# Performance work log

Hardware: AMD Instinct MI355X
Metric: run time of the kernel (lower is better)

## Reference

```python
import jax, jax.numpy as jnp
import numpy as np
import math

HIDDEN = 1024
N_HEADS = 16
HEAD_DIM = HIDDEN // N_HEADS
N_BLOCKS = 16
BATCH = 2
SEQ = 4096


def setup_inputs() -> dict:
    key = jax.random.key(0)
    ks = jax.random.split(key, 8)
    attention_input = jax.random.normal(ks[0], (BATCH, SEQ, HIDDEN), dtype=jnp.float32)
    attention_mask = jnp.ones((BATCH, SEQ), dtype=jnp.float32)
    # permutation over the num_blocks*num_heads flattened (block, head) axis
    permutation = jax.random.permutation(ks[1], N_BLOCKS * N_HEADS)
    init = 0.02
    q_w = jax.random.normal(ks[2], (HIDDEN, N_HEADS, HEAD_DIM), dtype=jnp.float32) * init
    q_b = jax.random.normal(ks[3], (N_HEADS, HEAD_DIM), dtype=jnp.float32) * init
    k_w = jax.random.normal(ks[4], (HIDDEN, N_HEADS, HEAD_DIM), dtype=jnp.float32) * init
    k_b = jax.random.normal(ks[5], (N_HEADS, HEAD_DIM), dtype=jnp.float32) * init
    v_w = jax.random.normal(ks[6], (HIDDEN, N_HEADS, HEAD_DIM), dtype=jnp.float32) * init
    v_b = jax.random.normal(ks[7], (N_HEADS, HEAD_DIM), dtype=jnp.float32) * init
    return {"attention_input": attention_input, "attention_mask": attention_mask,
            "permutation": permutation, "q_w": q_w, "q_b": q_b,
            "k_w": k_w, "k_b": k_b, "v_w": v_w, "v_b": v_b}


def reference(attention_input, attention_mask, permutation, q_w, q_b, k_w, k_b, v_w, v_b):
    B = attention_mask.shape[0]
    S = attention_mask.shape[1]
    nb = N_BLOCKS
    nh, d = q_b.shape
    blk = S // nb
    # QKV projections: [B,S,H] x [H,N,D] -> [B,S,N,D]
    q = jnp.einsum('bsh,hnd->bsnd', attention_input, q_w) + q_b
    k = jnp.einsum('bsh,hnd->bsnd', attention_input, k_w) + k_b
    v = jnp.einsum('bsh,hnd->bsnd', attention_input, v_w) + v_b

    def blockify(x):  # [B,S,N,D] -> [B, nb, nh, blk, d]
        return x.reshape(B, nb, blk, nh, d).transpose(0, 1, 3, 2, 4)

    q = blockify(q)
    # flatten (block, head) axis and gather per permutation
    k = blockify(k).reshape(B, nb * nh, blk, d)[:, permutation].reshape(B, nb, nh, blk, d)
    v = blockify(v).reshape(B, nb * nh, blk, d)[:, permutation].reshape(B, nb, nh, blk, d)

    scale = 1.0 / math.sqrt(float(d))
    logits = jnp.einsum('bgnqd,bgnkd->bgnqk', q, k) * scale  # block-local scores
    attn = jax.nn.softmax(logits, axis=-1)  # dropout prob 0 / eval mode
    ctx = jnp.einsum('bgnqk,bgnkd->bgnqd', attn, v)
    # [B,nb,nh,blk,d] -> [B,nb,blk,nh,d] -> [B,S,nh,d]
    return ctx.transpose(0, 1, 3, 2, 4).reshape(B, S, nh, d)
```

## Files before the change

### kernel.cpp

```cpp
#include <hip/hip_runtime.h>
#include <hip/hip_bf16.h>
#include <stdint.h>

#define HIDDEN 1024
#define NHEADS 16
#define HDIM   64
#define NBLK   16
#define BATCH  2
#define SEQ    4096
#define MTOT   (BATCH*SEQ)

typedef __attribute__((ext_vector_type(4))) float f32x4;
typedef __attribute__((ext_vector_type(8))) short s16x8;

__device__ inline short f2bf(float f) {
  union { float f; uint32_t u; } v; v.f = f;
  uint32_t r = v.u + 0x7fffu + ((v.u >> 16) & 1u);
  return (short)(r >> 16);
}

__device__ inline void gload_lds16(const void* g, void* l) {
  __builtin_amdgcn_global_load_lds((const __attribute__((address_space(1))) void*)g,
                                   (__attribute__((address_space(3))) void*)l,
                                   16, 0, 0);
}

__global__ __launch_bounds__(256) void k_convert_x(const float* __restrict__ x,
                                                   short* __restrict__ xb) {
  int i = (blockIdx.x * 256 + threadIdx.x) * 8;
  const float4* p = (const float4*)(x + i);
  float4 a = p[0], b = p[1];
  s16x8 o;
  o[0] = f2bf(a.x); o[1] = f2bf(a.y); o[2] = f2bf(a.z); o[3] = f2bf(a.w);
  o[4] = f2bf(b.x); o[5] = f2bf(b.y); o[6] = f2bf(b.z); o[7] = f2bf(b.w);
  *(s16x8*)(xb + i) = o;
}

__global__ __launch_bounds__(256) void k_transpose_w(const float* __restrict__ qw,
                                                     const float* __restrict__ kw,
                                                     const float* __restrict__ vw,
                                                     short* __restrict__ wt) {
  __shared__ float tile[64][65];
  int a  = blockIdx.x >> 8;
  int t2 = blockIdx.x & 255;
  int k0 = (t2 >> 4) << 6;
  int n0 = (t2 & 15) << 6;
  const float* w = (a == 0) ? qw : (a == 1) ? kw : vw;
  int c = threadIdx.x & 63, rr = threadIdx.x >> 6;
#pragma unroll
  for (int i = 0; i < 16; ++i) {
    int r = i * 4 + rr;
    tile[r][c] = w[(k0 + r) * 1024 + n0 + c];
  }
  __syncthreads();
  short* o = wt + a * 1048576;
#pragma unroll
  for (int i = 0; i < 16; ++i) {
    int r = i * 4 + rr;
    o[(n0 + r) * 1024 + k0 + c] = f2bf(tile[c][r]);
  }
}

__global__ __launch_bounds__(256) void k_gemm(const short* __restrict__ xb,
                                              const short* __restrict__ wt,
                                              const float* __restrict__ qbias,
                                              const float* __restrict__ kbias,
                                              const float* __restrict__ vbias,
                                              short* __restrict__ Qo,
                                              short* __restrict__ Ko,
                                              short* __restrict__ Vo) {
  __shared__ short As[128 * 64];
  __shared__ short Bs[128 * 64];
  int tid = threadIdx.x;
  int lane = tid & 63;
  int wv = tid >> 6;
  int mt = blockIdx.x, nt = blockIdx.y;
  int a = nt >> 3;
  const short* asrc = xb + (size_t)(mt * 128) * 1024;
  const short* bsrc = wt + (size_t)a * 1048576 + (size_t)((nt & 7) * 128) * 1024;

  f32x4 acc[4][4] = {};
  int wr = (wv >> 1) * 64, wc = (wv & 1) * 64;

  for (int kt = 0; kt < 16; ++kt) {
    int k0 = kt * 64;
#pragma unroll
    for (int i = 0; i < 4; ++i) {
      int c = i * 256 + tid;
      int row = c >> 3;
      int colb = (c & 7) << 4;
      int sc = colb ^ ((row & 7) << 4);
      gload_lds16(asrc + row * 1024 + k0 + (sc >> 1), (char*)As + c * 16);
      gload_lds16(bsrc + row * 1024 + k0 + (sc >> 1), (char*)Bs + c * 16);
    }
    __syncthreads();
#pragma unroll
    for (int ks = 0; ks < 2; ++ks) {
      s16x8 af[4], bfr[4];
      int cb = (ks << 6) + ((lane >> 4) << 4);
#pragma unroll
      for (int rf = 0; rf < 4; ++rf) {
        int row = wr + rf * 16 + (lane & 15);
        af[rf] = *(const s16x8*)((const char*)As + row * 128 + (cb ^ ((row & 7) << 4)));
      }
#pragma unroll
      for (int cf = 0; cf < 4; ++cf) {
        int row = wc + cf * 16 + (lane & 15);
        bfr[cf] = *(const s16x8*)((const char*)Bs + row * 128 + (cb ^ ((row & 7) << 4)));
      }
#pragma unroll
      for (int rf = 0; rf < 4; ++rf)
#pragma unroll
        for (int cf = 0; cf < 4; ++cf)
          acc[rf][cf] = __builtin_amdgcn_mfma_f32_16x16x32_bf16(af[rf], bfr[cf], acc[rf][cf], 0, 0, 0);
    }
    __syncthreads();
  }

  const float* bias = (a == 0) ? qbias : (a == 1) ? kbias : vbias;
  short* outp = (a == 0) ? Qo : (a == 1) ? Ko : Vo;
  int nbase = (nt & 7) * 128 + wc;
  int mbase = mt * 128 + wr;
#pragma unroll
  for (int cf = 0; cf < 4; ++cf) {
    int nloc = nbase + cf * 16 + (lane & 15);
    float bv = bias[nloc];
#pragma unroll
    for (int rf = 0; rf < 4; ++rf)
#pragma unroll
      for (int r = 0; r < 4; ++r) {
        int m = mbase + rf * 16 + ((lane >> 4) << 2) + r;
        outp[(size_t)m * 1024 + nloc] = f2bf(acc[rf][cf][r] + bv);
      }
  }
}

__global__ __launch_bounds__(512) void k_attn(const short* __restrict__ Qb,
                                              const short* __restrict__ Kb,
                                              const short* __restrict__ Vb,
                                              const int* __restrict__ perm,
                                              float* __restrict__ out) {
  __shared__ short Qs[256 * 64];
  __shared__ short Ks[256 * 64];
  __shared__ short Vs[64 * 256];
  __shared__ short Ps[8 * 1024];

  int tid = threadIdx.x;
  int lane = tid & 63, wv = tid >> 6;
  int bx = blockIdx.x;
  int b = bx >> 8, g = (bx >> 4) & 15, n = bx & 15;
  int p = perm[g * 16 + n];
  int pg = p >> 4, ph = p & 15;

  const short* qsrc = Qb + (size_t)(b * 4096 + g * 256) * 1024 + n * 64;
  const short* ksrc = Kb + (size_t)(b * 4096 + pg * 256) * 1024 + ph * 64;
  const short* vsrc = Vb + (size_t)(b * 4096 + pg * 256) * 1024 + ph * 64;

#pragma unroll
  for (int i = 0; i < 4; ++i) {
    int c = i * 512 + tid;
    int row = c >> 3;
    int colb = (c & 7) << 4;
    int sc = colb ^ ((row & 7) << 4);
    gload_lds16(qsrc + row * 1024 + (sc >> 1), (char*)Qs + c * 16);
    gload_lds16(ksrc + row * 1024 + (sc >> 1), (char*)Ks + c * 16);
  }
#pragma unroll
  for (int i = 0; i < 4; ++i) {
    int c = i * 512 + tid;
    int t = c >> 3;
    int d0 = (c & 7) << 3;
    s16x8 v = *(const s16x8*)(vsrc + t * 1024 + d0);
#pragma unroll
    for (int j = 0; j < 8; ++j) {
      int d = d0 + j;
      int by = d * 512 + ((t * 2) ^ ((d & 7) << 4));
      *(short*)((char*)Vs + by) = v[j];
    }
  }
  __syncthreads();

  int qr0 = wv * 32;
  f32x4 accS[2][16] = {};
#pragma unroll
  for (int ks = 0; ks < 2; ++ks) {
    int cb = (ks << 6) + ((lane >> 4) << 4);
    s16x8 aq[2];
#pragma unroll
    for (int rf = 0; rf < 2; ++rf) {
      int row = qr0 + rf * 16 + (lane & 15);
      aq[rf] = *(const s16x8*)((const char*)Qs + row * 128 + (cb ^ ((row & 7) << 4)));
    }
#pragma unroll
    for (int cf = 0; cf < 16; ++cf) {
      int row = cf * 16 + (lane & 15);
      s16x8 bk = *(const s16x8*)((const char*)Ks + row * 128 + (cb ^ ((row & 7) << 4)));
      accS[0][cf] = __builtin_amdgcn_mfma_f32_16x16x32_bf16(aq[0], bk, accS[0][cf], 0, 0, 0);
      accS[1][cf] = __builtin_amdgcn_mfma_f32_16x16x32_bf16(aq[1], bk, accS[1][cf], 0, 0, 0);
    }
  }

  const float sc_log2e = 0.125f * 1.44269504088896f;
  float mx[2][4], inv[2][4];
#pragma unroll
  for (int rf = 0; rf < 2; ++rf)
#pragma unroll
    for (int r = 0; r < 4; ++r) {
      float m_ = accS[rf][0][r];
#pragma unroll
      for (int cf = 1; cf < 16; ++cf) m_ = fmaxf(m_, accS[rf][cf][r]);
#pragma unroll
      for (int msk = 1; msk < 16; msk <<= 1) m_ = fmaxf(m_, __shfl_xor(m_, msk));
      mx[rf][r] = m_;
    }
#pragma unroll
  for (int rf = 0; rf < 2; ++rf)
#pragma unroll
    for (int r = 0; r < 4; ++r) {
      float s_ = 0.f;
#pragma unroll
      for (int cf = 0; cf < 16; ++cf) {
        float e = exp2f((accS[rf][cf][r] - mx[rf][r]) * sc_log2e);
        accS[rf][cf][r] = e;
        s_ += e;
      }
#pragma unroll
      for (int msk = 1; msk < 16; msk <<= 1) s_ += __shfl_xor(s_, msk);
      inv[rf][r] = 1.0f / s_;
    }

  f32x4 accO[2][4] = {};
  short* pchunk = Ps + wv * 1024;
#pragma unroll
  for (int ks = 0; ks < 8; ++ks) {
#pragma unroll
    for (int rf = 0; rf < 2; ++rf)
#pragma unroll
      for (int half = 0; half < 2; ++half) {
        int cf = ks * 2 + half;
        int kvl = half * 16 + (lane & 15);
        int qp = (lane >> 4) << 2;
        int base = rf * 512 + ((kvl >> 3) << 7) + (kvl & 7);
#pragma unroll
        for (int r = 0; r < 4; ++r)
          pchunk[base + (qp + r) * 8] = f2bf(accS[rf][cf][r]);
      }
    int cbv = (ks << 6) + ((lane >> 4) << 4);
#pragma unroll
    for (int rf = 0; rf < 2; ++rf) {
      s16x8 ap = *(const s16x8*)(pchunk + rf * 512 + lane * 8);
#pragma unroll
      for (int dc = 0; dc < 4; ++dc) {
        int vrow = dc * 16 + (lane & 15);
        s16x8 bv = *(const s16x8*)((const char*)Vs + vrow * 512 + (cbv ^ ((vrow & 7) << 4)));
        accO[rf][dc] = __builtin_amdgcn_mfma_f32_16x16x32_bf16(ap, bv, accO[rf][dc], 0, 0, 0);
      }
    }
  }

#pragma unroll
  for (int rf = 0; rf < 2; ++rf)
#pragma unroll
    for (int dc = 0; dc < 4; ++dc)
#pragma unroll
      for (int r = 0; r < 4; ++r) {
        int q = qr0 + rf * 16 + ((lane >> 4) << 2) + r;
        int d = dc * 16 + (lane & 15);
        out[(size_t)((b * 4096 + g * 256 + q) * 16 + n) * 64 + d] = accO[rf][dc][r] * inv[rf][r];
      }
}

extern "C" void kernel_launch(void* const* d_in, const int* in_sizes, int n_in,
                              void* d_out, int out_size, void* d_ws, size_t ws_size,
                              hipStream_t stream) {
  const float* x    = (const float*)d_in[0];
  const int*   perm = (const int*)d_in[2];
  const float* qw   = (const float*)d_in[3];
  const float* qb   = (const float*)d_in[4];
  const float* kw   = (const float*)d_in[5];
  const float* kb   = (const float*)d_in[6];
  const float* vw   = (const float*)d_in[7];
  const float* vb   = (const float*)d_in[8];
  float* out = (float*)d_out;

  char* ws = (char*)d_ws;
  short* Xb = (short*)(ws);
  short* Wt = (short*)(ws + 16777216UL);
  short* Qb = (short*)(ws + 23068672UL);
  short* Kb = (short*)(ws + 39845888UL);
  short* Vb = (short*)(ws + 56623104UL);

  k_convert_x<<<4096, 256, 0, stream>>>(x, Xb);
  k_transpose_w<<<768, 256, 0, stream>>>(qw, kw, vw, Wt);
  k_gemm<<<dim3(64, 24), 256, 0, stream>>>(Xb, Wt, qb, kb, vb, Qb, Kb, Vb);
  k_attn<<<512, 512, 0, stream>>>(Qb, Kb, Vb, perm, out);
}
```

Measured before the change: 113.9 us.

## Triple-buffer QKV GEMM with larger 256x128 tiles and direct Q loads in attention

Rewrites the QKV projection GEMM to use 256x128 block tiles with a K-step of 32 and a three-stage LDS ring. Prefetch now overlaps MFMA work through explicit vmcnt waits and raised wave priority, and a single barrier replaces the previous two per step. The attention kernel drops the Q staging in LDS and reads Q fragments directly from global memory, which lowers LDS use and may raise occupancy. The risks are higher register pressure from 32 accumulators per wave and uncoalesced direct global Q loads.

```diff
diff --git a/kernel.cpp b/kernel.cpp
--- a/kernel.cpp
+++ b/kernel.cpp
@@ -1,14 +1,6 @@
 #include <hip/hip_runtime.h>
 #include <hip/hip_bf16.h>
 #include <stdint.h>
-
-#define HIDDEN 1024
-#define NHEADS 16
-#define HDIM   64
-#define NBLK   16
-#define BATCH  2
-#define SEQ    4096
-#define MTOT   (BATCH*SEQ)
 
 typedef __attribute__((ext_vector_type(4))) float f32x4;
 typedef __attribute__((ext_vector_type(8))) short s16x8;
@@ -61,86 +53,131 @@
   }
 }
 
-__global__ __launch_bounds__(256) void k_gemm(const short* __restrict__ xb,
-                                              const short* __restrict__ wt,
-                                              const float* __restrict__ qbias,
-                                              const float* __restrict__ kbias,
-                                              const float* __restrict__ vbias,
-                                              short* __restrict__ Qo,
-                                              short* __restrict__ Ko,
-                                              short* __restrict__ Vo) {
-  __shared__ short As[128 * 64];
-  __shared__ short Bs[128 * 64];
-  int tid = threadIdx.x;
-  int lane = tid & 63;
-  int wv = tid >> 6;
-  int mt = blockIdx.x, nt = blockIdx.y;
-  int a = nt >> 3;
-  const short* asrc = xb + (size_t)(mt * 128) * 1024;
-  const short* bsrc = wt + (size_t)a * 1048576 + (size_t)((nt & 7) * 128) * 1024;
-
-  f32x4 acc[4][4] = {};
-  int wr = (wv >> 1) * 64, wc = (wv & 1) * 64;
-
-  for (int kt = 0; kt < 16; ++kt) {
-    int k0 = kt * 64;
-#pragma unroll
-    for (int i = 0; i < 4; ++i) {
-      int c = i * 256 + tid;
-      int row = c >> 3;
-      int colb = (c & 7) << 4;
-      int sc = colb ^ ((row & 7) << 4);
-      gload_lds16(asrc + row * 1024 + k0 + (sc >> 1), (char*)As + c * 16);
-      gload_lds16(bsrc + row * 1024 + k0 + (sc >> 1), (char*)Bs + c * 16);
-    }
-    __syncthreads();
-#pragma unroll
-    for (int ks = 0; ks < 2; ++ks) {
-      s16x8 af[4], bfr[4];
-      int cb = (ks << 6) + ((lane >> 4) << 4);
-#pragma unroll
-      for (int rf = 0; rf < 4; ++rf) {
-        int row = wr + rf * 16 + (lane & 15);
-        af[rf] = *(const s16x8*)((const char*)As + row * 128 + (cb ^ ((row & 7) << 4)));
-      }
-#pragma unroll
-      for (int cf = 0; cf < 4; ++cf) {
-        int row = wc + cf * 16 + (lane & 15);
-        bfr[cf] = *(const s16x8*)((const char*)Bs + row * 128 + (cb ^ ((row & 7) << 4)));
-      }
-#pragma unroll
-      for (int rf = 0; rf < 4; ++rf)
-#pragma unroll
-        for (int cf = 0; cf < 4; ++cf)
-          acc[rf][cf] = __builtin_amdgcn_mfma_f32_16x16x32_bf16(af[rf], bfr[cf], acc[rf][cf], 0, 0, 0);
-    }
-    __syncthreads();
+__global__ __launch_bounds__(256, 2) void k_gemm(const short* __restrict__ xb,
+                                                 const short* __restrict__ wt,
+                                                 const float* __restrict__ qbias,
+                                                 const float* __restrict__ kbias,
+                                                 const float* __restrict__ vbias,
+                                                 short* __restrict__ Qo,
+                                                 short* __restrict__ Ko,
+                                                 short* __restrict__ Vo) {
+  __shared__ short lds[36864];
+  const int tid = threadIdx.x, lane = tid & 63, wv = tid >> 6;
+  const int wm = wv >> 1, wn = wv & 1;
+  const int mt = blockIdx.x, by = blockIdx.y;
+  const int a = by >> 3;
+  const short* asrc = xb + (size_t)(mt * 256) * 1024;
+  const short* bsrc = wt + (size_t)a * 1048576 + (size_t)((by & 7) * 128) * 1024;
+
+  int srcA[4], dstA[4], srcB[2], dstB[2];
+#pragma unroll
+  for (int i = 0; i < 4; ++i) {
+    int L = i * 256 + tid, s = L & 31;
+    int row = (L >> 5) * 8 + (s >> 2);
+    int c = (s & 3) ^ ((s >> 3) & 3);
+    srcA[i] = row * 1024 + c * 8;
+    dstA[i] = L * 16;
+  }
+#pragma unroll
+  for (int i = 0; i < 2; ++i) {
+    int L = i * 256 + tid, s = L & 31;
+    int row = (L >> 5) * 8 + (s >> 2);
+    int c = (s & 3) ^ ((s >> 3) & 3);
+    srcB[i] = row * 1024 + c * 8;
+    dstB[i] = 16384 + L * 16;
+  }
+
+  int aoff[8], boff[4];
+#pragma unroll
+  for (int m = 0; m < 8; ++m) {
+    int row = wm * 128 + m * 16 + (lane & 15);
+    aoff[m] = ((row >> 3) * 32 + (row & 7) * 4 + ((lane >> 4) ^ ((row >> 1) & 3))) * 16;
+  }
+#pragma unroll
+  for (int n = 0; n < 4; ++n) {
+    int row = wn * 64 + n * 16 + (lane & 15);
+    boff[n] = 16384 + ((row >> 3) * 32 + (row & 7) * 4 + ((lane >> 4) ^ ((row >> 1) & 3))) * 16;
+  }
+
+  f32x4 acc[8][4] = {};
+
+  auto STAGE = [&](int t, int bb) {
+    const short* at = asrc + t * 32;
+    const short* bt = bsrc + t * 32;
+    char* l = (char*)lds + bb;
+#pragma unroll
+    for (int i = 0; i < 4; ++i) gload_lds16(at + srcA[i], l + dstA[i]);
+#pragma unroll
+    for (int i = 0; i < 2; ++i) gload_lds16(bt + srcB[i], l + dstB[i]);
+  };
+
+  STAGE(0, 0);
+  STAGE(1, 24576);
+  int bcur = 0, bpre = 49152;
+
+  for (int t = 0; t < 31; ++t) {
+    asm volatile("s_waitcnt vmcnt(6)" ::: "memory");
+    __builtin_amdgcn_s_barrier();
+    asm volatile("" ::: "memory");
+    if (t < 30) STAGE(t + 2, bpre);
+    const char* bufc = (const char*)lds + bcur;
+    s16x8 af[8], bf[4];
+#pragma unroll
+    for (int m = 0; m < 8; ++m) af[m] = *(const s16x8*)(bufc + aoff[m]);
+#pragma unroll
+    for (int n = 0; n < 4; ++n) bf[n] = *(const s16x8*)(bufc + boff[n]);
+    __builtin_amdgcn_s_setprio(1);
+#pragma unroll
+    for (int m = 0; m < 8; ++m)
+#pragma unroll
+      for (int n = 0; n < 4; ++n)
+        acc[m][n] = __builtin_amdgcn_mfma_f32_16x16x32_bf16(af[m], bf[n], acc[m][n], 0, 0, 0);
+    __builtin_amdgcn_s_setprio(0);
+    bcur += 24576; if (bcur == 73728) bcur = 0;
+    bpre += 24576; if (bpre == 73728) bpre = 0;
+  }
+  asm volatile("s_waitcnt vmcnt(0)" ::: "memory");
+  __builtin_amdgcn_s_barrier();
+  asm volatile("" ::: "memory");
+  {
+    const char* bufc = (const char*)lds + bcur;
+    s16x8 af[8], bf[4];
+#pragma unroll
+    for (int m = 0; m < 8; ++m) af[m] = *(const s16x8*)(bufc + aoff[m]);
+#pragma unroll
+    for (int n = 0; n < 4; ++n) bf[n] = *(const s16x8*)(bufc + boff[n]);
+    __builtin_amdgcn_s_setprio(1);
+#pragma unroll
+    for (int m = 0; m < 8; ++m)
+#pragma unroll
+      for (int n = 0; n < 4; ++n)
+        acc[m][n] = __builtin_amdgcn_mfma_f32_16x16x32_bf16(af[m], bf[n], acc[m][n], 0, 0, 0);
+    __builtin_amdgcn_s_setprio(0);
   }
 
   const float* bias = (a == 0) ? qbias : (a == 1) ? kbias : vbias;
   short* outp = (a == 0) ? Qo : (a == 1) ? Ko : Vo;
-  int nbase = (nt & 7) * 128 + wc;
-  int mbase = mt * 128 + wr;
-#pragma unroll
-  for (int cf = 0; cf < 4; ++cf) {
-    int nloc = nbase + cf * 16 + (lane & 15);
+  int nbase = (by & 7) * 128 + wn * 64;
+  int mbase = mt * 256 + wm * 128;
+#pragma unroll
+  for (int n = 0; n < 4; ++n) {
+    int nloc = nbase + n * 16 + (lane & 15);
     float bv = bias[nloc];
 #pragma unroll
-    for (int rf = 0; rf < 4; ++rf)
+    for (int m = 0; m < 8; ++m)
 #pragma unroll
       for (int r = 0; r < 4; ++r) {
-        int m = mbase + rf * 16 + ((lane >> 4) << 2) + r;
-        outp[(size_t)m * 1024 + nloc] = f2bf(acc[rf][cf][r] + bv);
-      }
-  }
-}
-
-__global__ __launch_bounds__(512) void k_attn(const short* __restrict__ Qb,
-                                              const short* __restrict__ Kb,
-                                              const short* __restrict__ Vb,
-                                              const int* __restrict__ perm,
-                                              float* __restrict__ out) {
-  __shared__ short Qs[256 * 64];
+        int mm = mbase + m * 16 + ((lane >> 4) << 2) + r;
+        outp[(size_t)mm * 1024 + nloc] = f2bf(acc[m][n][r] + bv);
+      }
+  }
+}
+
+__global__ void k_attn(const short* __restrict__ Qb,
+                       const short* __restrict__ Kb,
+                       const short* __restrict__ Vb,
+                       const int* __restrict__ perm,
+                       float* __restrict__ out) {
   __shared__ short Ks[256 * 64];
   __shared__ short Vs[64 * 256];
   __shared__ short Ps[8 * 1024];
@@ -162,7 +199,6 @@
     int row = c >> 3;
     int colb = (c & 7) << 4;
     int sc = colb ^ ((row & 7) << 4);
-    gload_lds16(qsrc + row * 1024 + (sc >> 1), (char*)Qs + c * 16);
     gload_lds16(ksrc + row * 1024 + (sc >> 1), (char*)Ks + c * 16);
   }
 #pragma unroll
@@ -189,7 +225,7 @@
 #pragma unroll
     for (int rf = 0; rf < 2; ++rf) {
       int row = qr0 + rf * 16 + (lane & 15);
-      aq[rf] = *(const s16x8*)((const char*)Qs + row * 128 + (cb ^ ((row & 7) << 4)));
+      aq[rf] = *(const s16x8*)(qsrc + row * 1024 + ks * 32 + ((lane >> 4) << 3));
     }
 #pragma unroll
     for (int cf = 0; cf < 16; ++cf) {
@@ -292,6 +328,6 @@
 
   k_convert_x<<<4096, 256, 0, stream>>>(x, Xb);
   k_transpose_w<<<768, 256, 0, stream>>>(qw, kw, vw, Wt);
-  k_gemm<<<dim3(64, 24), 256, 0, stream>>>(Xb, Wt, qb, kb, vb, Qb, Kb, Vb);
+  k_gemm<<<dim3(32, 24), 256, 0, stream>>>(Xb, Wt, qb, kb, vb, Qb, Kb, Vb);
   k_attn<<<512, 512, 0, stream>>>(Qb, Kb, Vb, perm, out);
 }
```

Result: slower. 199.7 us (+75.3%).
